# Kernel tuning notes

Hardware: AMD Instinct MI355X
Metric: run time of the kernel (lower is better)

Reference implementation:

```python
import jax, jax.numpy as jnp
import numpy as np

EMB = 128
HEADS = 8
B = 8
T = 2048


def setup_inputs() -> dict:
    key = jax.random.key(0)
    ks = jax.random.split(key, 6)
    x = jax.random.normal(ks[0], (B, T, EMB), dtype=jnp.float32)
    # torch Linear(emb, heads*emb, bias=False): store as (in, out) so y = x @ W
    scale = 1.0 / np.sqrt(EMB)
    Wq = jax.random.uniform(ks[1], (EMB, HEADS * EMB), jnp.float32, -scale, scale)
    Wk = jax.random.uniform(ks[2], (EMB, HEADS * EMB), jnp.float32, -scale, scale)
    Wv = jax.random.uniform(ks[3], (EMB, HEADS * EMB), jnp.float32, -scale, scale)
    so = 1.0 / np.sqrt(HEADS * EMB)
    Wo = jax.random.uniform(ks[4], (HEADS * EMB, EMB), jnp.float32, -so, so)
    bo = jax.random.uniform(ks[5], (EMB,), jnp.float32, -so, so)
    return {"x": x, "Wq": Wq, "Wk": Wk, "Wv": Wv, "Wo": Wo, "bo": bo}


def reference(x, Wq, Wk, Wv, Wo, bo):
    b, t, e = x.shape
    h = HEADS
    q = (x @ Wq).reshape(b, t, h, e)  # [b,t,h,e]
    k = (x @ Wk).reshape(b, t, h, e)
    v = (x @ Wv).reshape(b, t, h, e)
    # scores: [b,h,q,k], scaled by sqrt(e) (per-head dim == emb here)
    scores = jnp.einsum('bqhe,bkhe->bhqk', q, k) / jnp.sqrt(jnp.asarray(e, x.dtype))
    attn = jax.nn.softmax(scores, axis=-1)
    out = jnp.einsum('bhqk,bkhe->bqhe', attn, v).reshape(b, t, h * e)
    return out @ Wo + bo
```

## Files before the change

### kernel.cpp

```cpp
#include <hip/hip_runtime.h>

using bf16x8 = __attribute__((ext_vector_type(8))) short;
using f32x4  = __attribute__((ext_vector_type(4))) float;
using f32x16 = __attribute__((ext_vector_type(16))) float;

__device__ __forceinline__ ushort f2bf(float f) {
    union { float f; unsigned int u; } c; c.f = f;
    unsigned int u = c.u;
    u = (u + 0x7fffu + ((u >> 16) & 1u)) >> 16;
    return (ushort)u;
}

#if defined(__has_builtin)
#if __has_builtin(__builtin_amdgcn_cvt_pk_bf16_f32)
#define HAS_PK_BF16 1
#endif
#if __has_builtin(__builtin_amdgcn_permlane32_swap)
#define HAS_PL32 1
#endif
#endif
__device__ __forceinline__ unsigned int pkbf(float a, float b) {
#ifdef HAS_PK_BF16
    typedef __bf16 bf2 __attribute__((ext_vector_type(2)));
    union { bf2 v; unsigned int u; } cv;
    cv.v = __builtin_amdgcn_cvt_pk_bf16_f32(a, b);
    return cv.u;
#else
    return (unsigned int)f2bf(a) | ((unsigned int)f2bf(b) << 16);
#endif
}

__device__ __forceinline__ void pl32swap(unsigned &a, unsigned &b) {
#ifdef HAS_PL32
    typedef unsigned uint2v __attribute__((ext_vector_type(2)));
    uint2v r = __builtin_amdgcn_permlane32_swap(a, b, false, false);
    a = r.x; b = r.y;
#else
    asm volatile("v_permlane32_swap_b32 %0, %1" : "+v"(a), "+v"(b));
#endif
}

__device__ __forceinline__ void dma16(const ushort* g, ushort* l) {
    __builtin_amdgcn_global_load_lds(
        (const __attribute__((address_space(1))) unsigned int*)g,
        (__attribute__((address_space(3))) unsigned int*)l, 16, 0, 0);
}

constexpr int BB   = 8;
constexpr int HH   = 8;
constexpr int TT   = 2048;
constexpr int DD   = 128;
#define C2F (0.08838834764831845f * 1.4426950408889634f)

__global__ void prep_kernel(const float* __restrict__ x,
                            const float* __restrict__ Wq, const float* __restrict__ Wk,
                            const float* __restrict__ Wv, const float* __restrict__ Wo,
                            ushort* __restrict__ xb, ushort* __restrict__ WqkvT,
                            ushort* __restrict__ WoT) {
    int t = blockIdx.x * 256 + threadIdx.x;
    if (t < 524288) {
        float4 v = ((const float4*)x)[t];
        ushort4 o;
        o.x = f2bf(v.x); o.y = f2bf(v.y); o.z = f2bf(v.z); o.w = f2bf(v.w);
        ((ushort4*)xb)[t] = o;
    } else if (t < 524288 + 393216) {
        int i = t - 524288;
        int j = i >> 7, kk = i & 127;
        const float* W = (j < 1024) ? Wq : ((j < 2048) ? Wk : Wv);
        int jj = j & 1023;
        WqkvT[j * 128 + kk] = f2bf(W[kk * 1024 + jj]);
    } else {
        int i = t - 917504;
        int e = i >> 10, kk = i & 1023;
        WoT[e * 1024 + kk] = f2bf(Wo[kk * 128 + e]);
    }
}

__global__ __launch_bounds__(256, 2)
void qkv_gemm(const ushort* __restrict__ xb, const ushort* __restrict__ WqkvT,
              ushort* __restrict__ q, ushort* __restrict__ k, ushort* __restrict__ vt) {
    __shared__ ushort Al[128 * 136];
    __shared__ ushort Bl[128 * 136];
    const int tid = threadIdx.x;
    const int n0 = blockIdx.x * 128, m0 = blockIdx.y * 128;

    for (int s = tid; s < 2048; s += 256) {
        int row = s >> 4, oct = s & 15;
        *(uint4*)&Al[row * 136 + oct * 8] = *(const uint4*)&xb[m0 * 128 + s * 8];
        *(uint4*)&Bl[row * 136 + oct * 8] = *(const uint4*)&WqkvT[n0 * 128 + s * 8];
    }
    __syncthreads();

    const int w = tid >> 6, lane = tid & 63, l15 = lane & 15, g = lane >> 4;
    const int wm = (w & 1) * 64, wn = (w >> 1) * 64;
    f32x4 acc[4][4] = {};

#pragma unroll
    for (int ks = 0; ks < 4; ks++) {
        bf16x8 af[4], bfr[4];
#pragma unroll
        for (int mb = 0; mb < 4; mb++)
            af[mb] = *(const bf16x8*)&Al[(wm + mb * 16 + l15) * 136 + ks * 32 + g * 8];
#pragma unroll
        for (int nb = 0; nb < 4; nb++)
            bfr[nb] = *(const bf16x8*)&Bl[(wn + nb * 16 + l15) * 136 + ks * 32 + g * 8];
#pragma unroll
        for (int mb = 0; mb < 4; mb++)
#pragma unroll
            for (int nb = 0; nb < 4; nb++)
                acc[mb][nb] = __builtin_amdgcn_mfma_f32_16x16x32_bf16(af[mb], bfr[nb], acc[mb][nb], 0, 0, 0);
    }

    const int which = n0 >> 10;
    const int b = m0 >> 11;
    const int h = (n0 >> 7) & 7;
    const int bh = b * HH + h;
    if (which == 0) {
#pragma unroll
        for (int mb = 0; mb < 4; mb++)
#pragma unroll
            for (int nb = 0; nb < 4; nb++)
#pragma unroll
                for (int r = 0; r < 4; r++) {
                    int t = (m0 + wm + mb * 16 + g * 4 + r) & 2047;
                    int e = wn + nb * 16 + l15;
                    q[((size_t)bh * TT + t) * DD + e] = f2bf(acc[mb][nb][r] * C2F);
                }
    } else if (which == 1) {
#pragma unroll
        for (int mb = 0; mb < 4; mb++)
#pragma unroll
            for (int nb = 0; nb < 4; nb++)
#pragma unroll
                for (int r = 0; r < 4; r++) {
                    int t = (m0 + wm + mb * 16 + g * 4 + r) & 2047;
                    int e = wn + nb * 16 + l15;
                    int esw = ((((e >> 3) ^ (t & 7)) << 3) | (e & 7));
                    k[((size_t)bh * TT + t) * DD + esw] = f2bf(acc[mb][nb][r]);
                }
    } else {
        __syncthreads();
        ushort* Tl = Al;
#pragma unroll
        for (int mb = 0; mb < 4; mb++)
#pragma unroll
            for (int nb = 0; nb < 4; nb++)
#pragma unroll
                for (int r = 0; r < 4; r++)
                    Tl[(wn + nb * 16 + l15) * 136 + wm + mb * 16 + g * 4 + r] = f2bf(acc[mb][nb][r]);
        __syncthreads();
        const int c0 = (m0 & 2047) >> 5;
        for (int s = tid; s < 2048; s += 256) {
            int e = s >> 4, x = s & 15;
            int cl = x >> 2, pos = x & 3;
            int el = e & 15;
            int vsw = (el ^ (el >> 2)) & 3;
            int tsrc = cl * 32 + ((pos ^ vsw) * 8);
            uint4 val = *(const uint4*)&Tl[e * 136 + tsrc];
            *(uint4*)&vt[(size_t)(((bh * 64 + c0 + cl) * 128) + e) * 32 + pos * 8] = val;
        }
    }
}

__global__ __launch_bounds__(256, 2)
void attn_kernel(const ushort* __restrict__ q, const ushort* __restrict__ k,
                 const ushort* __restrict__ vt, ushort* __restrict__ ao) {
    __shared__ ushort Kl[2][32 * 128];
    __shared__ ushort Vl[2][128 * 32];

    const int idx = blockIdx.x;
    const int qt256 = idx & 7, h = (idx >> 3) & 7, b = idx >> 6;
    const int t0 = qt256 * 256;
    const int bh = b * HH + h;
    const ushort* qg  = q  + (size_t)bh * TT * DD;
    const ushort* kg  = k  + (size_t)bh * TT * DD;
    const ushort* vtg = vt + (size_t)bh * 64 * DD * 32;

    const int tid = threadIdx.x, w = tid >> 6, lane = tid & 63;
    const int l31 = lane & 31, hi = lane >> 5, l15 = lane & 15;
    const int swk = lane & 7;
    const int swv = (l15 ^ (l15 >> 2)) & 3;

    bf16x8 qf[2][8];
#pragma unroll
    for (int qt = 0; qt < 2; qt++)
#pragma unroll
        for (int ks = 0; ks < 8; ks++)
            qf[qt][ks] = *(const bf16x8*)&qg[(size_t)(t0 + w * 64 + qt * 32 + l31) * DD + ks * 16 + hi * 8];

    const int seg = tid * 8;
#pragma unroll
    for (int j = 0; j < 2; j++) {
        dma16(kg  + seg + j * 2048, &Kl[0][seg + j * 2048]);
        dma16(vtg + seg + j * 2048, &Vl[0][seg + j * 2048]);
    }

    f32x16 o[2][4] = {};
    float ls[2] = {0.0f, 0.0f};

    for (int c = 0; c < 64; c++) {
        const int cur = c & 1;
        __syncthreads();

        if (c < 63) {
            const ushort* kn = kg  + (size_t)(c + 1) * 4096;
            const ushort* vn = vtg + (size_t)(c + 1) * 4096;
#pragma unroll
            for (int j = 0; j < 2; j++) {
                dma16(kn + seg + j * 2048, &Kl[cur ^ 1][seg + j * 2048]);
                dma16(vn + seg + j * 2048, &Vl[cur ^ 1][seg + j * 2048]);
            }
        }

        f32x16 st0 = {}, st1 = {};
        __builtin_amdgcn_s_setprio(1);
#pragma unroll
        for (int ks = 0; ks < 8; ks++) {
            bf16x8 kf = *(const bf16x8*)&Kl[cur][l31 * 128 + (((ks * 2 + hi) ^ swk) * 8)];
            st0 = __builtin_amdgcn_mfma_f32_32x32x16_bf16(kf, qf[0][ks], st0, 0, 0, 0);
            st1 = __builtin_amdgcn_mfma_f32_32x32x16_bf16(kf, qf[1][ks], st1, 0, 0, 0);
        }
        __builtin_amdgcn_s_setprio(0);

        bf16x8 pa00, pa01, pa10, pa11;
        auto sm = [&](const f32x16 st, float& lsr, bf16x8& paA, bf16x8& paB) {
            float p[16];
#pragma unroll
            for (int r = 0; r < 16; r++) p[r] = __builtin_amdgcn_exp2f(st[r]);
            lsr += (((p[0] + p[1]) + (p[2] + p[3])) + ((p[4] + p[5]) + (p[6] + p[7])))
                 + (((p[8] + p[9]) + (p[10] + p[11])) + ((p[12] + p[13]) + (p[14] + p[15])));
            unsigned a0 = pkbf(p[0],  p[1]),  a1 = pkbf(p[2],  p[3]);
            unsigned a2 = pkbf(p[4],  p[5]),  a3 = pkbf(p[6],  p[7]);
            unsigned a4 = pkbf(p[8],  p[9]),  a5 = pkbf(p[10], p[11]);
            unsigned a6 = pkbf(p[12], p[13]), a7 = pkbf(p[14], p[15]);
            pl32swap(a0, a2); pl32swap(a1, a3);
            pl32swap(a4, a6); pl32swap(a5, a7);
            union { unsigned u[4]; bf16x8 v; } A, B;
            A.u[0] = a0; A.u[1] = a1; A.u[2] = a2; A.u[3] = a3;
            B.u[0] = a4; B.u[1] = a5; B.u[2] = a6; B.u[3] = a7;
            paA = A.v; paB = B.v;
        };
        sm(st0, ls[0], pa00, pa01);
        sm(st1, ls[1], pa10, pa11);

        __builtin_amdgcn_s_setprio(1);
#pragma unroll
        for (int et = 0; et < 4; et++) {
#pragma unroll
            for (int ks2 = 0; ks2 < 2; ks2++) {
                bf16x8 vb = *(const bf16x8*)&Vl[cur][(et * 32 + l31) * 32 + (((ks2 * 2 + hi) ^ swv) * 8)];
                o[0][et] = __builtin_amdgcn_mfma_f32_32x32x16_bf16(ks2 ? pa01 : pa00, vb, o[0][et], 0, 0, 0);
                o[1][et] = __builtin_amdgcn_mfma_f32_32x32x16_bf16(ks2 ? pa11 : pa10, vb, o[1][et], 0, 0, 0);
            }
        }
        __builtin_amdgcn_s_setprio(0);
    }

    const size_t aobase = (size_t)(b * TT) * 1024 + h * 128;
#pragma unroll
    for (int qt = 0; qt < 2; qt++) {
        float tot = ls[qt] + __shfl_xor(ls[qt], 32);
#pragma unroll
        for (int r = 0; r < 16; r++) {
            int ql = (r & 3) + 8 * (r >> 2) + 4 * hi;
            float inv = 1.0f / __shfl(tot, ql, 64);
            int m = t0 + w * 64 + qt * 32 + ql;
#pragma unroll
            for (int et = 0; et < 4; et++)
                ao[aobase + (size_t)m * 1024 + et * 32 + l31] = f2bf(o[qt][et][r] * inv);
        }
    }
}

__global__ __launch_bounds__(256, 2)
void outproj_gemm(const ushort* __restrict__ ao, const ushort* __restrict__ WoT,
                  const float* __restrict__ bo, float* __restrict__ out) {
    __shared__ ushort Al[64 * 72];
    __shared__ ushort Bl[64 * 72];
    const int tid = threadIdx.x;
    const int n0 = blockIdx.x * 64, m0 = blockIdx.y * 64;
    const int w = tid >> 6, lane = tid & 63, l15 = lane & 15, g = lane >> 4;
    const int wm = (w & 1) * 32, wn = (w >> 1) * 32;
    f32x4 acc[2][2] = {};

    for (int kc = 0; kc < 16; kc++) {
        int k0 = kc * 64;
        __syncthreads();
        for (int s = tid; s < 512; s += 256) {
            int row = s >> 3, oct = s & 7;
            *(uint4*)&Al[row * 72 + oct * 8] = *(const uint4*)&ao[(size_t)(m0 + row) * 1024 + k0 + oct * 8];
            *(uint4*)&Bl[row * 72 + oct * 8] = *(const uint4*)&WoT[(n0 + row) * 1024 + k0 + oct * 8];
        }
        __syncthreads();
#pragma unroll
        for (int ks = 0; ks < 2; ks++) {
            bf16x8 af[2], bfr[2];
#pragma unroll
            for (int mb = 0; mb < 2; mb++)
                af[mb] = *(const bf16x8*)&Al[(wm + mb * 16 + l15) * 72 + ks * 32 + g * 8];
#pragma unroll
            for (int nb = 0; nb < 2; nb++)
                bfr[nb] = *(const bf16x8*)&Bl[(wn + nb * 16 + l15) * 72 + ks * 32 + g * 8];
#pragma unroll
            for (int mb = 0; mb < 2; mb++)
#pragma unroll
                for (int nb = 0; nb < 2; nb++)
                    acc[mb][nb] = __builtin_amdgcn_mfma_f32_16x16x32_bf16(af[mb], bfr[nb], acc[mb][nb], 0, 0, 0);
        }
    }

#pragma unroll
    for (int mb = 0; mb < 2; mb++)
#pragma unroll
        for (int nb = 0; nb < 2; nb++) {
            int j = n0 + wn + nb * 16 + l15;
            float bias = bo[j];
#pragma unroll
            for (int r = 0; r < 4; r++) {
                int m = m0 + wm + mb * 16 + g * 4 + r;
                out[(size_t)m * 128 + j] = acc[mb][nb][r] + bias;
            }
        }
}

extern "C" void kernel_launch(void* const* d_in, const int* in_sizes, int n_in,
                              void* d_out, int out_size, void* d_ws, size_t ws_size,
                              hipStream_t stream) {
    const float* x  = (const float*)d_in[0];
    const float* Wq = (const float*)d_in[1];
    const float* Wk = (const float*)d_in[2];
    const float* Wv = (const float*)d_in[3];
    const float* Wo = (const float*)d_in[4];
    const float* bo = (const float*)d_in[5];
    float* out = (float*)d_out;

    char* ws = (char*)d_ws;
    ushort* xb    = (ushort*)(ws);
    ushort* WqkvT = (ushort*)(ws + 4194304);
    ushort* WoT   = (ushort*)(ws + 4980736);
    ushort* qb    = (ushort*)(ws + 5242880);
    ushort* kb    = (ushort*)(ws + 38797312);
    ushort* vtb   = (ushort*)(ws + 72351744);
    ushort* ao    = (ushort*)(ws + 105906176);

    prep_kernel<<<4096, 256, 0, stream>>>(x, Wq, Wk, Wv, Wo, xb, WqkvT, WoT);
    qkv_gemm<<<dim3(24, 128), 256, 0, stream>>>(xb, WqkvT, qb, kb, vtb);
    attn_kernel<<<512, 256, 0, stream>>>(qb, kb, vtb, ao);
    outproj_gemm<<<dim3(2, 256), 256, 0, stream>>>(ao, WoT, bo, out);
}
```

Measured before the change: 271.7 us.

## Halve attention query tile, triple-buffer K/V with explicit vmcnt waits, reorder blocks

```diff
diff --git a/kernel.cpp b/kernel.cpp
--- a/kernel.cpp
+++ b/kernel.cpp
@@ -162,15 +162,15 @@
     }
 }
 
-__global__ __launch_bounds__(256, 2)
+__global__ __launch_bounds__(256, 3)
 void attn_kernel(const ushort* __restrict__ q, const ushort* __restrict__ k,
                  const ushort* __restrict__ vt, ushort* __restrict__ ao) {
-    __shared__ ushort Kl[2][32 * 128];
-    __shared__ ushort Vl[2][128 * 32];
+    __shared__ ushort Kl[3][32 * 128];
+    __shared__ ushort Vl[3][128 * 32];
 
     const int idx = blockIdx.x;
-    const int qt256 = idx & 7, h = (idx >> 3) & 7, b = idx >> 6;
-    const int t0 = qt256 * 256;
+    const int h = idx & 7, b = (idx >> 3) & 7, qt128 = idx >> 6;
+    const int t0 = qt128 * 128;
     const int bh = b * HH + h;
     const ushort* qg  = q  + (size_t)bh * TT * DD;
     const ushort* kg  = k  + (size_t)bh * TT * DD;
@@ -181,67 +181,64 @@
     const int swk = lane & 7;
     const int swv = (l15 ^ (l15 >> 2)) & 3;
 
-    bf16x8 qf[2][8];
-#pragma unroll
-    for (int qt = 0; qt < 2; qt++)
-#pragma unroll
-        for (int ks = 0; ks < 8; ks++)
-            qf[qt][ks] = *(const bf16x8*)&qg[(size_t)(t0 + w * 64 + qt * 32 + l31) * DD + ks * 16 + hi * 8];
+    bf16x8 qf[8];
+#pragma unroll
+    for (int ks = 0; ks < 8; ks++)
+        qf[ks] = *(const bf16x8*)&qg[(size_t)(t0 + w * 32 + l31) * DD + ks * 16 + hi * 8];
 
     const int seg = tid * 8;
 #pragma unroll
-    for (int j = 0; j < 2; j++) {
-        dma16(kg  + seg + j * 2048, &Kl[0][seg + j * 2048]);
-        dma16(vtg + seg + j * 2048, &Vl[0][seg + j * 2048]);
-    }
-
-    f32x16 o[2][4] = {};
-    float ls[2] = {0.0f, 0.0f};
-
+    for (int pc = 0; pc < 2; pc++)
+#pragma unroll
+        for (int j = 0; j < 2; j++) {
+            dma16(kg  + (size_t)pc * 4096 + seg + j * 2048, &Kl[pc][seg + j * 2048]);
+            dma16(vtg + (size_t)pc * 4096 + seg + j * 2048, &Vl[pc][seg + j * 2048]);
+        }
+
+    f32x16 o[4] = {};
+    float ls = 0.0f;
+
+    int cur = 0, nxt = 2;
     for (int c = 0; c < 64; c++) {
-        const int cur = c & 1;
-        __syncthreads();
-
-        if (c < 63) {
-            const ushort* kn = kg  + (size_t)(c + 1) * 4096;
-            const ushort* vn = vtg + (size_t)(c + 1) * 4096;
+        if (c < 63) asm volatile("s_waitcnt vmcnt(4)" ::: "memory");
+        else        asm volatile("s_waitcnt vmcnt(0)" ::: "memory");
+        __builtin_amdgcn_s_barrier();
+        __builtin_amdgcn_sched_barrier(0);
+
+        if (c < 62) {
+            const ushort* kn = kg  + (size_t)(c + 2) * 4096;
+            const ushort* vn = vtg + (size_t)(c + 2) * 4096;
 #pragma unroll
             for (int j = 0; j < 2; j++) {
-                dma16(kn + seg + j * 2048, &Kl[cur ^ 1][seg + j * 2048]);
-                dma16(vn + seg + j * 2048, &Vl[cur ^ 1][seg + j * 2048]);
+                dma16(kn + seg + j * 2048, &Kl[nxt][seg + j * 2048]);
+                dma16(vn + seg + j * 2048, &Vl[nxt][seg + j * 2048]);
             }
         }
 
-        f32x16 st0 = {}, st1 = {};
+        f32x16 st = {};
         __builtin_amdgcn_s_setprio(1);
 #pragma unroll
         for (int ks = 0; ks < 8; ks++) {
             bf16x8 kf = *(const bf16x8*)&Kl[cur][l31 * 128 + (((ks * 2 + hi) ^ swk) * 8)];
-            st0 = __builtin_amdgcn_mfma_f32_32x32x16_bf16(kf, qf[0][ks], st0, 0, 0, 0);
-            st1 = __builtin_amdgcn_mfma_f32_32x32x16_bf16(kf, qf[1][ks], st1, 0, 0, 0);
+            st = __builtin_amdgcn_mfma_f32_32x32x16_bf16(kf, qf[ks], st, 0, 0, 0);
         }
         __builtin_amdgcn_s_setprio(0);
 
-        bf16x8 pa00, pa01, pa10, pa11;
-        auto sm = [&](const f32x16 st, float& lsr, bf16x8& paA, bf16x8& paB) {
-            float p[16];
-#pragma unroll
-            for (int r = 0; r < 16; r++) p[r] = __builtin_amdgcn_exp2f(st[r]);
-            lsr += (((p[0] + p[1]) + (p[2] + p[3])) + ((p[4] + p[5]) + (p[6] + p[7])))
-                 + (((p[8] + p[9]) + (p[10] + p[11])) + ((p[12] + p[13]) + (p[14] + p[15])));
-            unsigned a0 = pkbf(p[0],  p[1]),  a1 = pkbf(p[2],  p[3]);
-            unsigned a2 = pkbf(p[4],  p[5]),  a3 = pkbf(p[6],  p[7]);
-            unsigned a4 = pkbf(p[8],  p[9]),  a5 = pkbf(p[10], p[11]);
-            unsigned a6 = pkbf(p[12], p[13]), a7 = pkbf(p[14], p[15]);
-            pl32swap(a0, a2); pl32swap(a1, a3);
-            pl32swap(a4, a6); pl32swap(a5, a7);
-            union { unsigned u[4]; bf16x8 v; } A, B;
-            A.u[0] = a0; A.u[1] = a1; A.u[2] = a2; A.u[3] = a3;
-            B.u[0] = a4; B.u[1] = a5; B.u[2] = a6; B.u[3] = a7;
-            paA = A.v; paB = B.v;
-        };
-        sm(st0, ls[0], pa00, pa01);
-        sm(st1, ls[1], pa10, pa11);
+        float p[16];
+#pragma unroll
+        for (int r = 0; r < 16; r++) p[r] = __builtin_amdgcn_exp2f(st[r]);
+        ls += (((p[0] + p[1]) + (p[2] + p[3])) + ((p[4] + p[5]) + (p[6] + p[7])))
+            + (((p[8] + p[9]) + (p[10] + p[11])) + ((p[12] + p[13]) + (p[14] + p[15])));
+        unsigned a0 = pkbf(p[0],  p[1]),  a1 = pkbf(p[2],  p[3]);
+        unsigned a2 = pkbf(p[4],  p[5]),  a3 = pkbf(p[6],  p[7]);
+        unsigned a4 = pkbf(p[8],  p[9]),  a5 = pkbf(p[10], p[11]);
+        unsigned a6 = pkbf(p[12], p[13]), a7 = pkbf(p[14], p[15]);
+        pl32swap(a0, a2); pl32swap(a1, a3);
+        pl32swap(a4, a6); pl32swap(a5, a7);
+        union { unsigned u[4]; bf16x8 v; } A, B;
+        A.u[0] = a0; A.u[1] = a1; A.u[2] = a2; A.u[3] = a3;
+        B.u[0] = a4; B.u[1] = a5; B.u[2] = a6; B.u[3] = a7;
+        bf16x8 paA = A.v, paB = B.v;
 
         __builtin_amdgcn_s_setprio(1);
 #pragma unroll
@@ -249,26 +246,25 @@
 #pragma unroll
             for (int ks2 = 0; ks2 < 2; ks2++) {
                 bf16x8 vb = *(const bf16x8*)&Vl[cur][(et * 32 + l31) * 32 + (((ks2 * 2 + hi) ^ swv) * 8)];
-                o[0][et] = __builtin_amdgcn_mfma_f32_32x32x16_bf16(ks2 ? pa01 : pa00, vb, o[0][et], 0, 0, 0);
-                o[1][et] = __builtin_amdgcn_mfma_f32_32x32x16_bf16(ks2 ? pa11 : pa10, vb, o[1][et], 0, 0, 0);
+                o[et] = __builtin_amdgcn_mfma_f32_32x32x16_bf16(ks2 ? paB : paA, vb, o[et], 0, 0, 0);
             }
         }
         __builtin_amdgcn_s_setprio(0);
-    }
-
+
+        cur = (cur == 2) ? 0 : cur + 1;
+        nxt = (nxt == 2) ? 0 : nxt + 1;
+    }
+
+    float tot = ls + __shfl_xor(ls, 32);
     const size_t aobase = (size_t)(b * TT) * 1024 + h * 128;
 #pragma unroll
-    for (int qt = 0; qt < 2; qt++) {
-        float tot = ls[qt] + __shfl_xor(ls[qt], 32);
-#pragma unroll
-        for (int r = 0; r < 16; r++) {
-            int ql = (r & 3) + 8 * (r >> 2) + 4 * hi;
-            float inv = 1.0f / __shfl(tot, ql, 64);
-            int m = t0 + w * 64 + qt * 32 + ql;
-#pragma unroll
-            for (int et = 0; et < 4; et++)
-                ao[aobase + (size_t)m * 1024 + et * 32 + l31] = f2bf(o[qt][et][r] * inv);
-        }
+    for (int r = 0; r < 16; r++) {
+        int ql = (r & 3) + 8 * (r >> 2) + 4 * hi;
+        float inv = 1.0f / __shfl(tot, ql, 64);
+        int m = t0 + w * 32 + ql;
+#pragma unroll
+        for (int et = 0; et < 4; et++)
+            ao[aobase + (size_t)m * 1024 + et * 32 + l31] = f2bf(o[et][r] * inv);
     }
 }
 
@@ -345,6 +341,6 @@
 
     prep_kernel<<<4096, 256, 0, stream>>>(x, Wq, Wk, Wv, Wo, xb, WqkvT, WoT);
     qkv_gemm<<<dim3(24, 128), 256, 0, stream>>>(xb, WqkvT, qb, kb, vtb);
-    attn_kernel<<<512, 256, 0, stream>>>(qb, kb, vtb, ao);
+    attn_kernel<<<1024, 256, 0, stream>>>(qb, kb, vtb, ao);
     outproj_gemm<<<dim3(2, 256), 256, 0, stream>>>(ao, WoT, bo, out);
 }
```

Result: slower. 283.1 us (+4.2%).
